# Optimization experiments

Hardware: AMD Instinct MI355X
Metric: run time of the kernel (lower is better)

The kernel has to match this reference:

```python
import jax, jax.numpy as jnp
import numpy as np

B, T, HOR, N = 32, 12, 12, 883
D = 10      # embed_dim == time_dim
HID = 64    # rnn_units
OUT = 1     # output_dim
K = 2       # cheb_k: supports [I, A]


def _pdg2(x, e1, e2, E, Wp, bp):
    # x:[B,N,Ci]  e1,e2:[B,N,D]  E:[N,D]  Wp:[D,K,Ci,Co]  bp:[D,Co]
    nv1 = jnp.tanh(E[None] * e1)                      # [B,N,D]
    nv2 = jnp.tanh(E[None] * e2)
    A = jax.nn.softmax(jax.nn.relu(jnp.einsum('bnd,bmd->bnm', nv1, nv2)), axis=-1)
    xg = jnp.stack([x, jnp.einsum('bnm,bmc->bnc', A, x)], axis=2)   # [B,N,K,Ci]
    W = jnp.einsum('bnd,dkio->bnkio', nv1, Wp)        # node/time-adaptive weights
    b = jnp.einsum('bnd,do->bno', nv1, bp)
    return jnp.einsum('bnki,bnkio->bno', xg, W) + b


def _cell(x, h, e1, e2, E, gW, gb, uW, ub):
    xs = jnp.concatenate([x, h], axis=-1)
    zr = jax.nn.sigmoid(_pdg2(xs, e1, e2, E, gW, gb))
    z, r = jnp.split(zr, 2, axis=-1)
    cand = jnp.concatenate([x, z * h], axis=-1)
    hc = jnp.tanh(_pdg2(cand, e1, e2, E, uW, ub))
    return r * h + (1.0 - r) * hc


def setup_inputs() -> dict:
    key = jax.random.key(0)
    ks = jax.random.split(key, 20)
    s = 0.1
    inp = {
        'src_vals': jax.random.normal(ks[0], (B, T, N, 1), jnp.float32),
        'node_emb': s * jax.random.normal(ks[1], (N, D), jnp.float32),
        'tid_emb1': s * jax.random.normal(ks[2], (288, D), jnp.float32),
        'tid_emb2': s * jax.random.normal(ks[3], (288, D), jnp.float32),
        'diw_emb1': s * jax.random.normal(ks[4], (7, D), jnp.float32),
        'diw_emb2': s * jax.random.normal(ks[5], (7, D), jnp.float32),
        'enc_gate_W': s * jax.random.normal(ks[6], (D, K, 1 + HID, 2 * HID), jnp.float32),
        'enc_gate_b': s * jax.random.normal(ks[7], (D, 2 * HID), jnp.float32),
        'enc_upd_W': s * jax.random.normal(ks[8], (D, K, 1 + HID, HID), jnp.float32),
        'enc_upd_b': s * jax.random.normal(ks[9], (D, HID), jnp.float32),
        'dec_gate_W': s * jax.random.normal(ks[10], (D, K, OUT + HID, 2 * HID), jnp.float32),
        'dec_gate_b': s * jax.random.normal(ks[11], (D, 2 * HID), jnp.float32),
        'dec_upd_W': s * jax.random.normal(ks[12], (D, K, OUT + HID, HID), jnp.float32),
        'dec_upd_b': s * jax.random.normal(ks[13], (D, HID), jnp.float32),
        'proj_W': s * jax.random.normal(ks[14], (OUT, HID), jnp.float32),
        'proj_b': jnp.zeros((OUT,), jnp.float32),
        'src_tid': jax.random.randint(ks[15], (B, T, N), 0, 288, jnp.int32),
        'src_diw': jax.random.randint(ks[16], (B, T, N), 0, 7, jnp.int32),
        'tgt_tid': jax.random.randint(ks[17], (B, HOR, N), 0, 288, jnp.int32),
        'tgt_diw': jax.random.randint(ks[18], (B, HOR, N), 0, 7, jnp.int32),
    }
    return inp


def reference(src_vals, node_emb, tid_emb1, tid_emb2, diw_emb1, diw_emb2,
              enc_gate_W, enc_gate_b, enc_upd_W, enc_upd_b,
              dec_gate_W, dec_gate_b, dec_upd_W, dec_upd_b,
              proj_W, proj_b, src_tid, src_diw, tgt_tid, tgt_diw):
    tm = lambda a: jnp.swapaxes(a, 0, 1)   # batch-major -> time-major
    # periodic embeddings (use_week=True -> elementwise product)
    e1_en = tid_emb1[src_tid] * diw_emb1[src_diw]   # [B,T,N,D]
    e2_en = tid_emb2[src_tid] * diw_emb2[src_diw]
    e1_de = tid_emb1[tgt_tid] * diw_emb1[tgt_diw]   # [B,HOR,N,D]
    e2_de = tid_emb2[tgt_tid] * diw_emb2[tgt_diw]

    h0 = jnp.zeros((src_vals.shape[0], node_emb.shape[0], HID), src_vals.dtype)

    def enc_step(h, inp):
        x, e1, e2 = inp
        h = _cell(x, h, e1, e2, node_emb, enc_gate_W, enc_gate_b, enc_upd_W, enc_upd_b)
        return h, None

    h, _ = jax.lax.scan(enc_step, h0, (tm(src_vals), tm(e1_en), tm(e2_en)))

    go0 = jnp.zeros((src_vals.shape[0], node_emb.shape[0], OUT), src_vals.dtype)

    def dec_step(carry, inp):
        h, go = carry
        e1, e2 = inp
        h = _cell(go, h, e1, e2, node_emb, dec_gate_W, dec_gate_b, dec_upd_W, dec_upd_b)
        go = h @ proj_W.T + proj_b
        return (h, go), go

    _, outs = jax.lax.scan(dec_step, (h, go0), (tm(e1_de), tm(e2_de)))
    return jnp.swapaxes(outs, 0, 1)   # [B,HOR,N,OUT]
```

## Files before the change

kernel.cpp:

```cpp
#include <hip/hip_runtime.h>

#define BB 32
#define TSRC 12
#define HORZ 12
#define NN 883
#define DD 10
#define HH 64
#define BN (BB*NN)
#define BNP 28288
#define KF 5
#define NT 14

typedef __attribute__((ext_vector_type(8))) short short8;
typedef __attribute__((ext_vector_type(4))) float f32x4;

static __device__ __forceinline__ float sigmf(float x) { return 1.f/(1.f + __expf(-x)); }
static __device__ __forceinline__ float tanh_fast(float x) {
  float e = __expf(2.f*x);
  return (e - 1.f) / (e + 1.f);
}
static __device__ __forceinline__ unsigned int bf_hi(float f) {
  unsigned int u = __float_as_uint(f);
  return (u + 0x7fffu + ((u >> 16) & 1u)) >> 16;
}
static __device__ __forceinline__ float bf_f(unsigned int h) {
  return __uint_as_float(h << 16);
}
static __device__ __forceinline__ void lds_load16(const void* g, void* l) {
  __builtin_amdgcn_global_load_lds(
      (const __attribute__((address_space(1))) void*)g,
      (__attribute__((address_space(3))) void*)l, 16, 0, 0);
}

static __device__ __forceinline__ void swz_block(int& b, int& rt) {
  int lin = blockIdx.x + blockIdx.y*NT;
  int c = lin & 7, q = lin >> 3;
  b = c + ((q/NT) << 3);
  rt = q - (q/NT)*NT;
}

static __device__ __forceinline__ void xs_store(unsigned short* chunk, int c, int mm2, float v) {
  int p0 = (c*128 + (mm2 ^ ((c & 7) << 4))) >> 1;
  unsigned int hi = bf_hi(v);
  chunk[p0] = (unsigned short)hi;
  chunk[p0 + 4096] = (unsigned short)bf_hi(v - bf_f(hi));
}

__global__ __launch_bounds__(256) void prep_kernel(
    const float* __restrict__ tidE1, const float* __restrict__ tidE2,
    const float* __restrict__ diwE1, const float* __restrict__ diwE2,
    const float* __restrict__ nodeE,
    const int* __restrict__ tididx, const int* __restrict__ diwidx,
    const float* __restrict__ xsrc, int xmode, int t, int tlen,
    float* __restrict__ nv1T, float* __restrict__ nv2T,
    unsigned short* __restrict__ XsH, unsigned short* __restrict__ XsZ)
{
  int i = blockIdx.x*256 + threadIdx.x;
  if (i >= BN) return;
  int b = i / NN, n = i - b*NN;
  int gi = (b*tlen + t)*NN + n;
  int ti = tididx[gi]*DD, di = diwidx[gi]*DD;
  int nE = n*DD;
#pragma unroll
  for (int d = 0; d < DD; ++d) {
    float E = nodeE[nE+d];
    nv1T[d*BNP+i] = tanh_fast(E * (tidE1[ti+d] * diwE1[di+d]));
    nv2T[d*BNP+i] = tanh_fast(E * (tidE2[ti+d] * diwE2[di+d]));
  }
  float xv = (xmode == 0) ? xsrc[gi] : xsrc[i];
  size_t cb = ((size_t)(b*NT + (n >> 6)))*8192;
  int mm = n & 63;
  unsigned int hi = bf_hi(xv);
  unsigned short los = (unsigned short)bf_hi(xv - bf_f(hi));
  XsH[cb + mm] = (unsigned short)hi; XsH[cb + 4096 + mm] = los;
  XsZ[cb + mm] = (unsigned short)hi; XsZ[cb + 4096 + mm] = los;
}

__global__ __launch_bounds__(256) void wsplit_kernel(
    const float* __restrict__ W, const float* __restrict__ bias,
    int NO, unsigned short* __restrict__ Wf)
{
  int i = blockIdx.x*256 + threadIdx.x;
  int total = DD*2*KF*4*NO*8;
  if (i >= total) return;
  int j = i & 7; int r = i >> 3;
  int o = r % NO; r /= NO;
  int quad = r & 3; r >>= 2;
  int kf = r % KF; r /= KF;
  int hl = r & 1; int d = r >> 1;
  int kk = kf*32 + quad*8 + j;
  float v = 0.f;
  if (kk <= 64)       v = W[(size_t)(d*130 + kk)*NO + o];
  else if (kk == 65)  v = bias[d*NO + o];
  else if (kk <= 130) v = W[(size_t)(d*130 + kk - 1)*NO + o];
  unsigned int hi = bf_hi(v);
  Wf[i] = (hl == 0) ? (unsigned short)hi : (unsigned short)bf_hi(v - bf_f(hi));
}


__global__ __launch_bounds__(256,3) void attn_gate(
    const float* __restrict__ nv1T, const float* __restrict__ nv2T,
    const unsigned short* __restrict__ Xs,
    const float* __restrict__ hsrc,
    const float* __restrict__ xsrc, int xmode, int t, int tlen,
    const unsigned short* __restrict__ Wf,
    float* __restrict__ zh, float* __restrict__ rbuf,
    unsigned short* __restrict__ XsZ)
{
  __shared__ float nv1s[DD][64];
  __shared__ float linv[64];
  __shared__ alignas(16) unsigned char U[46080];
  unsigned short* XT = (unsigned short*)U;
  unsigned short* PT = (unsigned short*)(U + 16384);
  float* nv2s = (float*)(U + 34816);
  float* xcolb = (float*)(U + 39936);
  int b, rt;
  swz_block(b, rt);
  int r0 = rt*64;
  int tid = threadIdx.x;
  int rg = tid >> 4, cg = tid & 15;
  int base = b*NN;
  int lane = tid & 63, lm = lane & 15, quad = lane >> 4;
  int w = tid >> 6, mp = w >> 1, np = w & 1;
  const unsigned short* XsB = Xs + (size_t)b*NT*8192;

  for (int idx = tid; idx < DD*64; idx += 256) {
    int d = idx >> 6, r = idx & 63;
    nv1s[d][r] = (r0 + r < NN) ? nv1T[d*BNP + base + r0 + r] : 0.f;
  }

  int4 xt[4];
  float nvr[3]; float xcr;
  {
    const int4* s0 = (const int4*)XsB;
#pragma unroll
    for (int i = 0; i < 4; ++i) xt[i] = s0[w*64 + lane + i*256];
#pragma unroll
    for (int i = 0; i < 3; ++i) {
      int idx = tid + i*256; float v = 0.f;
      if (idx < DD*64) { int d = idx>>6, m = idx&63; v = (m < NN) ? nv2T[d*BNP + base + m] : 0.f; }
      nvr[i] = v;
    }
    xcr = (tid < 64 && tid < NN) ? hsrc[(size_t)63*BNP + base + tid] : 0.f;
#pragma unroll
    for (int i = 0; i < 4; ++i)
      *(int4*)((char*)XT + w*1024 + lane*16 + i*4096) = xt[i];
#pragma unroll
    for (int i = 0; i < 3; ++i) {
      int idx = tid + i*256;
      if (idx < DD*64) nv2s[idx] = nvr[i];
    }
    if (tid < 64) xcolb[tid] = xcr;
  }
  __syncthreads();

  f32x4 accv[2][2] = {};
  float acclp[4] = {}, acc5p[4] = {};

  for (int tI = 0; tI < NT; ++tI) {
    int cur = tI & 1, nxt = cur ^ 1;
    int m0 = tI*64, m0n = m0 + 64;
    bool hasn = tI < NT-1;
    if (hasn) {
      const int4* src = (const int4*)(XsB + (size_t)(tI+1)*8192);
#pragma unroll
      for (int i = 0; i < 4; ++i) xt[i] = src[w*64 + lane + i*256];
#pragma unroll
      for (int i = 0; i < 3; ++i) {
        int idx = tid + i*256; float v = 0.f;
        if (idx < DD*64) { int d = idx>>6, m = idx&63; v = (m0n + m < NN) ? nv2T[d*BNP + base + m0n + m] : 0.f; }
        nvr[i] = v;
      }
      xcr = (tid < 64 && m0n + tid < NN) ? hsrc[(size_t)63*BNP + base + m0n + tid] : 0.f;
    }
    float s[4][4] = {};
#pragma unroll
    for (int d = 0; d < DD; ++d) {
      float4 a4 = *(const float4*)&nv1s[d][rg*4];
      float4 c4 = *(const float4*)&nv2s[cur*(DD*64) + d*64 + cg*4];
      const float* ap = (const float*)&a4;
      const float* cp = (const float*)&c4;
#pragma unroll
      for (int j = 0; j < 4; ++j)
#pragma unroll
        for (int jj = 0; jj < 4; ++jj)
          s[j][jj] += ap[j]*cp[jj];
    }
    int mvlim = NN - m0;
    float ev[4][4];
#pragma unroll
    for (int jj = 0; jj < 4; ++jj) {
      int m = cg*4 + jj;
      float xm = xcolb[cur*64 + m];
      bool okm = m < mvlim;
#pragma unroll
      for (int j = 0; j < 4; ++j) {
        float e = okm ? __expf(fmaxf(s[j][jj], 0.f)) : 0.f;
        ev[j][jj] = e;
        acclp[j] += e;
        acc5p[j] = fmaf(e, xm, acc5p[j]);
      }
    }
    {
      unsigned int* P1 = (unsigned int*)PT;
      unsigned int* P2 = (unsigned int*)(PT + 64*72);
#pragma unroll
      for (int j = 0; j < 4; ++j) {
        int r = rg*4 + j;
        unsigned int h0 = bf_hi(ev[j][0]), h1 = bf_hi(ev[j][1]), h2 = bf_hi(ev[j][2]), h3 = bf_hi(ev[j][3]);
        unsigned int l0 = bf_hi(ev[j][0]-bf_f(h0)), l1 = bf_hi(ev[j][1]-bf_f(h1));
        unsigned int l2 = bf_hi(ev[j][2]-bf_f(h2)), l3 = bf_hi(ev[j][3]-bf_f(h3));
        int dw = r*36 + cg*2;
        P1[dw] = h0 | (h1 << 16); P1[dw+1] = h2 | (h3 << 16);
        P2[dw] = l0 | (l1 << 16); P2[dw+1] = l2 | (l3 << 16);
      }
    }
    __syncthreads();
    {
      short8 Aa[2][2], Ab[2][2], Ba[2][2], Bb[2][2];
#pragma unroll
      for (int mt = 0; mt < 2; ++mt) {
        int r = mp*32 + mt*16 + lm;
#pragma unroll
        for (int kf = 0; kf < 2; ++kf) {
          Aa[mt][kf] = *(const short8*)&PT[r*72 + quad*8 + kf*32];
          Ab[mt][kf] = *(const short8*)&PT[64*72 + r*72 + quad*8 + kf*32];
        }
      }
#pragma unroll
      for (int ntl = 0; ntl < 2; ++ntl) {
        int c = np*32 + ntl*16 + lm;
        int swz = (c & 7) << 4;
        int cb0 = c*128 + quad*16;
#pragma unroll
        for (int kf = 0; kf < 2; ++kf) {
          int a = (cb0 + kf*64) ^ swz;
          Ba[ntl][kf] = *(const short8*)((const char*)XT + a);
          Bb[ntl][kf] = *(const short8*)((const char*)XT + a + 8192);
        }
      }
#pragma unroll
      for (int kf = 0; kf < 2; ++kf)
#pragma unroll
        for (int mt = 0; mt < 2; ++mt)
#pragma unroll
          for (int ntl = 0; ntl < 2; ++ntl) {
            accv[mt][ntl] = __builtin_amdgcn_mfma_f32_16x16x32_bf16(Aa[mt][kf], Ba[ntl][kf], accv[mt][ntl], 0,0,0);
            accv[mt][ntl] = __builtin_amdgcn_mfma_f32_16x16x32_bf16(Aa[mt][kf], Bb[ntl][kf], accv[mt][ntl], 0,0,0);
            accv[mt][ntl] = __builtin_amdgcn_mfma_f32_16x16x32_bf16(Ab[mt][kf], Ba[ntl][kf], accv[mt][ntl], 0,0,0);
          }
    }
    if (hasn) {
#pragma unroll
      for (int i = 0; i < 3; ++i) {
        int idx = tid + i*256;
        if (idx < DD*64) nv2s[nxt*(DD*64) + idx] = nvr[i];
      }
      if (tid < 64) xcolb[nxt*64 + tid] = xcr;
    }
    __syncthreads();
    if (hasn) {
#pragma unroll
      for (int i = 0; i < 4; ++i)
        *(int4*)((char*)XT + w*1024 + lane*16 + i*4096) = xt[i];
    }
  }
  int mrow_x = tid >> 2, ksub = tid & 3;
  int gmx = base + r0 + mrow_x;
  float hv0[9], hv1[9];
  {
    bool nok = (r0 + mrow_x) < NN;
    float xv;
    if (xmode == 0) xv = nok ? xsrc[(b*tlen+t)*NN + r0 + mrow_x] : 0.f;
    else xv = xsrc[gmx];
#pragma unroll
    for (int i = 0; i < 9; ++i) {
      int kk = ksub*2 + 8*i;
      if (kk > 64) { hv0[i] = 0.f; hv1[i] = 0.f; continue; }
      hv0[i] = (kk == 0) ? xv : hsrc[(size_t)(kk-1)*BNP + gmx];
      hv1[i] = (kk == 64) ? 1.f : hsrc[(size_t)kk*BNP + gmx];
    }
  }
#pragma unroll
  for (int off = 1; off <= 8; off <<= 1)
#pragma unroll
    for (int j = 0; j < 4; ++j) {
      acclp[j] += __shfl_xor(acclp[j], off, 64);
      acc5p[j] += __shfl_xor(acc5p[j], off, 64);
    }
  __syncthreads();
  {
    unsigned int* Z = (unsigned int*)(U + 36864);
    for (int idx = tid; idx < 2304; idx += 256) Z[idx] = 0;
  }
  __syncthreads();
  unsigned short* XA = (unsigned short*)U;
  if (cg == 0) {
#pragma unroll
    for (int j = 0; j < 4; ++j) {
      float li = 1.f / acclp[j];
      int r = rg*4 + j;
      linv[r] = li;
      float v = acc5p[j]*li;
      unsigned int hi = bf_hi(v);
      XA[(4*64 + r)*72 + 2] = (unsigned short)hi;
      XA[(4*64 + r)*72 + 32 + 2] = (unsigned short)bf_hi(v - bf_f(hi));
    }
  }
  __syncthreads();
#pragma unroll
  for (int mt = 0; mt < 2; ++mt) {
    int rbase = mp*32 + mt*16 + quad*4;
    float4 lv = *(const float4*)&linv[rbase];
    const float* lvp = (const float*)&lv;
#pragma unroll
    for (int ntl = 0; ntl < 2; ++ntl) {
      int c = np*32 + ntl*16 + lm;
      int kk = 66 + c;
      int kf = kk >> 5, kkl = kk & 31;
#pragma unroll
      for (int r4 = 0; r4 < 4; ++r4) {
        float v = accv[mt][ntl][r4] * lvp[r4];
        unsigned int hi = bf_hi(v);
        int p = (kf*64 + rbase + r4)*72 + kkl;
        XA[p] = (unsigned short)hi;
        XA[p + 32] = (unsigned short)bf_hi(v - bf_f(hi));
      }
    }
  }
  {
    unsigned int* X1 = (unsigned int*)U;
#pragma unroll
    for (int i = 0; i < 9; ++i) {
      int kk = ksub*2 + 8*i;
      if (kk > 64) continue;
      float v0 = hv0[i], v1 = hv1[i];
      unsigned int h0 = bf_hi(v0), h1 = bf_hi(v1);
      unsigned int l0 = bf_hi(v0 - bf_f(h0)), l1 = bf_hi(v1 - bf_f(h1));
      int kf = kk >> 5, kkl = kk & 31;
      int dw = (kf*64 + mrow_x)*36 + (kkl >> 1);
      X1[dw] = h0 | (h1 << 16);
      X1[dw + 16] = l0 | (l1 << 16);
    }
  }
  __syncthreads();
  short8 A1[2][KF], A2[2][KF];
#pragma unroll
  for (int mt = 0; mt < 2; ++mt) {
    int mrow = mp*32 + mt*16 + lm;
#pragma unroll
    for (int kf = 0; kf < KF; ++kf) {
      A1[mt][kf] = *(const short8*)&XA[(kf*64 + mrow)*72 + quad*8];
      A2[mt][kf] = *(const short8*)&XA[(kf*64 + mrow)*72 + 32 + quad*8];
    }
  }
  __syncthreads();
  unsigned char* bufA = U;
  unsigned char* bufB = U + 20480;
  const int colb = np*32 + lm;
#pragma unroll 1
  for (int co = 0; co < 2; ++co) {
    int co0 = co*64;
    {
      const unsigned short* src = Wf + ((size_t)(w*5)*128 + co0)*8 + lane*8;
#pragma unroll
      for (int i = 0; i < 5; ++i)
        lds_load16(src + (size_t)i*128*8, bufA + (w*5+i)*1024);
    }
    f32x4 accO[2][2] = {};
#pragma unroll 1
    for (int d = 0; d < DD; ++d) {
      f32x4 td[2][2] = {};
      __syncthreads();
      {
        const unsigned short* src = Wf + ((size_t)((d*2+1)*20 + w*5)*128 + co0)*8 + lane*8;
#pragma unroll
        for (int i = 0; i < 5; ++i)
          lds_load16(src + (size_t)i*128*8, bufB + (w*5+i)*1024);
      }
#pragma unroll
      for (int kf = 0; kf < KF; ++kf) {
        int cb = ((kf*4 + quad)*64 + colb)*16;
#pragma unroll
        for (int ntl = 0; ntl < 2; ++ntl) {
          short8 Bh = *(const short8*)(bufA + cb + ntl*256);
          td[0][ntl] = __builtin_amdgcn_mfma_f32_16x16x32_bf16(A1[0][kf], Bh, td[0][ntl], 0,0,0);
          td[0][ntl] = __builtin_amdgcn_mfma_f32_16x16x32_bf16(A2[0][kf], Bh, td[0][ntl], 0,0,0);
          td[1][ntl] = __builtin_amdgcn_mfma_f32_16x16x32_bf16(A1[1][kf], Bh, td[1][ntl], 0,0,0);
          td[1][ntl] = __builtin_amdgcn_mfma_f32_16x16x32_bf16(A2[1][kf], Bh, td[1][ntl], 0,0,0);
        }
      }
      __syncthreads();
      if (d < DD-1) {
        const unsigned short* src = Wf + ((size_t)((d+1)*2*20 + w*5)*128 + co0)*8 + lane*8;
#pragma unroll
        for (int i = 0; i < 5; ++i)
          lds_load16(src + (size_t)i*128*8, bufA + (w*5+i)*1024);
      }
#pragma unroll
      for (int kf = 0; kf < KF; ++kf) {
        int cb = ((kf*4 + quad)*64 + colb)*16;
#pragma unroll
        for (int ntl = 0; ntl < 2; ++ntl) {
          short8 Bl = *(const short8*)(bufB + cb + ntl*256);
          td[0][ntl] = __builtin_amdgcn_mfma_f32_16x16x32_bf16(A1[0][kf], Bl, td[0][ntl], 0,0,0);
          td[1][ntl] = __builtin_amdgcn_mfma_f32_16x16x32_bf16(A1[1][kf], Bl, td[1][ntl], 0,0,0);
        }
      }
#pragma unroll
      for (int mt = 0; mt < 2; ++mt) {
        float4 nv4 = *(const float4*)&nv1s[d][mp*32 + mt*16 + quad*4];
        const float* nvp = (const float*)&nv4;
#pragma unroll
        for (int ntl = 0; ntl < 2; ++ntl)
#pragma unroll
          for (int r = 0; r < 4; ++r)
            accO[mt][ntl][r] += nvp[r] * td[mt][ntl][r];
      }
    }
    float* CT = (float*)U;
    __syncthreads();
#pragma unroll
    for (int mt = 0; mt < 2; ++mt)
#pragma unroll
      for (int ntl = 0; ntl < 2; ++ntl)
#pragma unroll
        for (int r = 0; r < 4; ++r)
          CT[(mp*32 + mt*16 + quad*4 + r)*67 + np*32 + ntl*16 + lm] = accO[mt][ntl][r];
    __syncthreads();
    {
      int mm = tid & 63, og = tid >> 6;
      int n = r0 + mm;
      int gm = base + n;
      bool okn = n < NN;
      if (co == 0) {
        unsigned short* chk = XsZ + ((size_t)(b*NT + rt))*8192;
        int mm2 = mm*2;
        for (int j = 0; j < 16; ++j) {
          int o = og*16 + j;
          float z = sigmf(CT[mm*67 + o]);
          float zhv = z * hsrc[(size_t)o*BNP + gm];
          if (okn) {
            zh[(size_t)o*BNP + gm] = zhv;
            if (o < 63) xs_store(chk, o + 1, mm2, zhv);
          }
        }
      } else {
        for (int j = 0; j < 16; ++j) {
          int o = og*16 + j;
          if (okn) rbuf[(size_t)o*BNP + gm] = sigmf(CT[mm*67 + o]);
        }
      }
    }
    __syncthreads();
  }
}

__global__ __launch_bounds__(256,3) void attn_upd(
    const float* __restrict__ nv1T, const float* __restrict__ nv2T,
    const unsigned short* __restrict__ Xs,
    const float* __restrict__ hsrc,
    const float* __restrict__ hstate,
    const float* __restrict__ xsrc, int xmode, int t, int tlen,
    const unsigned short* __restrict__ Wf,
    const float* __restrict__ rbuf,
    int dec, const float* __restrict__ pW, const float* __restrict__ pb,
    float* __restrict__ go, float* __restrict__ dout,
    unsigned short* __restrict__ XsH)
{
  __shared__ float nv1s[DD][64];
  __shared__ float linv[64];
  __shared__ alignas(16) unsigned char U[46080];
  unsigned short* XT = (unsigned short*)U;
  unsigned short* PT = (unsigned short*)(U + 16384);
  float* nv2s = (float*)(U + 34816);
  float* xcolb = (float*)(U + 39936);
  int b, rt;
  swz_block(b, rt);
  int r0 = rt*64;
  int tid = threadIdx.x;
  int rg = tid >> 4, cg = tid & 15;
  int base = b*NN;
  int lane = tid & 63, lm = lane & 15, quad = lane >> 4;
  int w = tid >> 6, mp = w >> 1, np = w & 1;
  const unsigned short* XsB = Xs + (size_t)b*NT*8192;

  for (int idx = tid; idx < DD*64; idx += 256) {
    int d = idx >> 6, r = idx & 63;
    nv1s[d][r] = (r0 + r < NN) ? nv1T[d*BNP + base + r0 + r] : 0.f;
  }

  int4 xt[4];
  float nvr[3]; float xcr;
  {
    const int4* s0 = (const int4*)XsB;
#pragma unroll
    for (int i = 0; i < 4; ++i) xt[i] = s0[w*64 + lane + i*256];
#pragma unroll
    for (int i = 0; i < 3; ++i) {
      int idx = tid + i*256; float v = 0.f;
      if (idx < DD*64) { int d = idx>>6, m = idx&63; v = (m < NN) ? nv2T[d*BNP + base + m] : 0.f; }
      nvr[i] = v;
    }
    xcr = (tid < 64 && tid < NN) ? hsrc[(size_t)63*BNP + base + tid] : 0.f;
#pragma unroll
    for (int i = 0; i < 4; ++i)
      *(int4*)((char*)XT + w*1024 + lane*16 + i*4096) = xt[i];
#pragma unroll
    for (int i = 0; i < 3; ++i) {
      int idx = tid + i*256;
      if (idx < DD*64) nv2s[idx] = nvr[i];
    }
    if (tid < 64) xcolb[tid] = xcr;
  }
  __syncthreads();

  f32x4 accv[2][2] = {};
  float acclp[4] = {}, acc5p[4] = {};

  for (int tI = 0; tI < NT; ++tI) {
    int cur = tI & 1, nxt = cur ^ 1;
    int m0 = tI*64, m0n = m0 + 64;
    bool hasn = tI < NT-1;
    if (hasn) {
      const int4* src = (const int4*)(XsB + (size_t)(tI+1)*8192);
#pragma unroll
      for (int i = 0; i < 4; ++i) xt[i] = src[w*64 + lane + i*256];
#pragma unroll
      for (int i = 0; i < 3; ++i) {
        int idx = tid + i*256; float v = 0.f;
        if (idx < DD*64) { int d = idx>>6, m = idx&63; v = (m0n + m < NN) ? nv2T[d*BNP + base + m0n + m] : 0.f; }
        nvr[i] = v;
      }
      xcr = (tid < 64 && m0n + tid < NN) ? hsrc[(size_t)63*BNP + base + m0n + tid] : 0.f;
    }
    float s[4][4] = {};
#pragma unroll
    for (int d = 0; d < DD; ++d) {
      float4 a4 = *(const float4*)&nv1s[d][rg*4];
      float4 c4 = *(const float4*)&nv2s[cur*(DD*64) + d*64 + cg*4];
      const float* ap = (const float*)&a4;
      const float* cp = (const float*)&c4;
#pragma unroll
      for (int j = 0; j < 4; ++j)
#pragma unroll
        for (int jj = 0; jj < 4; ++jj)
          s[j][jj] += ap[j]*cp[jj];
    }
    int mvlim = NN - m0;
    float ev[4][4];
#pragma unroll
    for (int jj = 0; jj < 4; ++jj) {
      int m = cg*4 + jj;
      float xm = xcolb[cur*64 + m];
      bool okm = m < mvlim;
#pragma unroll
      for (int j = 0; j < 4; ++j) {
        float e = okm ? __expf(fmaxf(s[j][jj], 0.f)) : 0.f;
        ev[j][jj] = e;
        acclp[j] += e;
        acc5p[j] = fmaf(e, xm, acc5p[j]);
      }
    }
    {
      unsigned int* P1 = (unsigned int*)PT;
      unsigned int* P2 = (unsigned int*)(PT + 64*72);
#pragma unroll
      for (int j = 0; j < 4; ++j) {
        int r = rg*4 + j;
        unsigned int h0 = bf_hi(ev[j][0]), h1 = bf_hi(ev[j][1]), h2 = bf_hi(ev[j][2]), h3 = bf_hi(ev[j][3]);
        unsigned int l0 = bf_hi(ev[j][0]-bf_f(h0)), l1 = bf_hi(ev[j][1]-bf_f(h1));
        unsigned int l2 = bf_hi(ev[j][2]-bf_f(h2)), l3 = bf_hi(ev[j][3]-bf_f(h3));
        int dw = r*36 + cg*2;
        P1[dw] = h0 | (h1 << 16); P1[dw+1] = h2 | (h3 << 16);
        P2[dw] = l0 | (l1 << 16); P2[dw+1] = l2 | (l3 << 16);
      }
    }
    __syncthreads();
    {
      short8 Aa[2][2], Ab[2][2], Ba[2][2], Bb[2][2];
#pragma unroll
      for (int mt = 0; mt < 2; ++mt) {
        int r = mp*32 + mt*16 + lm;
#pragma unroll
        for (int kf = 0; kf < 2; ++kf) {
          Aa[mt][kf] = *(const short8*)&PT[r*72 + quad*8 + kf*32];
          Ab[mt][kf] = *(const short8*)&PT[64*72 + r*72 + quad*8 + kf*32];
        }
      }
#pragma unroll
      for (int ntl = 0; ntl < 2; ++ntl) {
        int c = np*32 + ntl*16 + lm;
        int swz = (c & 7) << 4;
        int cb0 = c*128 + quad*16;
#pragma unroll
        for (int kf = 0; kf < 2; ++kf) {
          int a = (cb0 + kf*64) ^ swz;
          Ba[ntl][kf] = *(const short8*)((const char*)XT + a);
          Bb[ntl][kf] = *(const short8*)((const char*)XT + a + 8192);
        }
      }
#pragma unroll
      for (int kf = 0; kf < 2; ++kf)
#pragma unroll
        for (int mt = 0; mt < 2; ++mt)
#pragma unroll
          for (int ntl = 0; ntl < 2; ++ntl) {
            accv[mt][ntl] = __builtin_amdgcn_mfma_f32_16x16x32_bf16(Aa[mt][kf], Ba[ntl][kf], accv[mt][ntl], 0,0,0);
            accv[mt][ntl] = __builtin_amdgcn_mfma_f32_16x16x32_bf16(Aa[mt][kf], Bb[ntl][kf], accv[mt][ntl], 0,0,0);
            accv[mt][ntl] = __builtin_amdgcn_mfma_f32_16x16x32_bf16(Ab[mt][kf], Ba[ntl][kf], accv[mt][ntl], 0,0,0);
          }
    }
    if (hasn) {
#pragma unroll
      for (int i = 0; i < 3; ++i) {
        int idx = tid + i*256;
        if (idx < DD*64) nv2s[nxt*(DD*64) + idx] = nvr[i];
      }
      if (tid < 64) xcolb[nxt*64 + tid] = xcr;
    }
    __syncthreads();
    if (hasn) {
#pragma unroll
      for (int i = 0; i < 4; ++i)
        *(int4*)((char*)XT + w*1024 + lane*16 + i*4096) = xt[i];
    }
  }
  int mrow_x = tid >> 2, ksub = tid & 3;
  int gmx = base + r0 + mrow_x;
  float hv0[9], hv1[9];
  {
    bool nok = (r0 + mrow_x) < NN;
    float xv;
    if (xmode == 0) xv = nok ? xsrc[(b*tlen+t)*NN + r0 + mrow_x] : 0.f;
    else xv = xsrc[gmx];
#pragma unroll
    for (int i = 0; i < 9; ++i) {
      int kk = ksub*2 + 8*i;
      if (kk > 64) { hv0[i] = 0.f; hv1[i] = 0.f; continue; }
      hv0[i] = (kk == 0) ? xv : hsrc[(size_t)(kk-1)*BNP + gmx];
      hv1[i] = (kk == 64) ? 1.f : hsrc[(size_t)kk*BNP + gmx];
    }
  }
#pragma unroll
  for (int off = 1; off <= 8; off <<= 1)
#pragma unroll
    for (int j = 0; j < 4; ++j) {
      acclp[j] += __shfl_xor(acclp[j], off, 64);
      acc5p[j] += __shfl_xor(acc5p[j], off, 64);
    }
  __syncthreads();
  {
    unsigned int* Z = (unsigned int*)(U + 36864);
    for (int idx = tid; idx < 2304; idx += 256) Z[idx] = 0;
  }
  __syncthreads();
  unsigned short* XA = (unsigned short*)U;
  if (cg == 0) {
#pragma unroll
    for (int j = 0; j < 4; ++j) {
      float li = 1.f / acclp[j];
      int r = rg*4 + j;
      linv[r] = li;
      float v = acc5p[j]*li;
      unsigned int hi = bf_hi(v);
      XA[(4*64 + r)*72 + 2] = (unsigned short)hi;
      XA[(4*64 + r)*72 + 32 + 2] = (unsigned short)bf_hi(v - bf_f(hi));
    }
  }
  __syncthreads();
#pragma unroll
  for (int mt = 0; mt < 2; ++mt) {
    int rbase = mp*32 + mt*16 + quad*4;
    float4 lv = *(const float4*)&linv[rbase];
    const float* lvp = (const float*)&lv;
#pragma unroll
    for (int ntl = 0; ntl < 2; ++ntl) {
      int c = np*32 + ntl*16 + lm;
      int kk = 66 + c;
      int kf = kk >> 5, kkl = kk & 31;
#pragma unroll
      for (int r4 = 0; r4 < 4; ++r4) {
        float v = accv[mt][ntl][r4] * lvp[r4];
        unsigned int hi = bf_hi(v);
        int p = (kf*64 + rbase + r4)*72 + kkl;
        XA[p] = (unsigned short)hi;
        XA[p + 32] = (unsigned short)bf_hi(v - bf_f(hi));
      }
    }
  }
  {
    unsigned int* X1 = (unsigned int*)U;
#pragma unroll
    for (int i = 0; i < 9; ++i) {
      int kk = ksub*2 + 8*i;
      if (kk > 64) continue;
      float v0 = hv0[i], v1 = hv1[i];
      unsigned int h0 = bf_hi(v0), h1 = bf_hi(v1);
      unsigned int l0 = bf_hi(v0 - bf_f(h0)), l1 = bf_hi(v1 - bf_f(h1));
      int kf = kk >> 5, kkl = kk & 31;
      int dw = (kf*64 + mrow_x)*36 + (kkl >> 1);
      X1[dw] = h0 | (h1 << 16);
      X1[dw + 16] = l0 | (l1 << 16);
    }
  }
  __syncthreads();
  short8 A1[2][KF], A2[2][KF];
#pragma unroll
  for (int mt = 0; mt < 2; ++mt) {
    int mrow = mp*32 + mt*16 + lm;
#pragma unroll
    for (int kf = 0; kf < KF; ++kf) {
      A1[mt][kf] = *(const short8*)&XA[(kf*64 + mrow)*72 + quad*8];
      A2[mt][kf] = *(const short8*)&XA[(kf*64 + mrow)*72 + 32 + quad*8];
    }
  }
  __syncthreads();
  unsigned char* bufA = U;
  unsigned char* bufB = U + 20480;
  const int colb = np*32 + lm;
  {
    const unsigned short* src = Wf + (size_t)(w*5)*64*8 + lane*8;
#pragma unroll
    for (int i = 0; i < 5; ++i)
      lds_load16(src + (size_t)i*64*8, bufA + (w*5+i)*1024);
  }
  f32x4 accO[2][2] = {};
#pragma unroll 1
  for (int d = 0; d < DD; ++d) {
    f32x4 td[2][2] = {};
    __syncthreads();
    {
      const unsigned short* src = Wf + (size_t)((d*2+1)*20 + w*5)*64*8 + lane*8;
#pragma unroll
      for (int i = 0; i < 5; ++i)
        lds_load16(src + (size_t)i*64*8, bufB + (w*5+i)*1024);
    }
#pragma unroll
    for (int kf = 0; kf < KF; ++kf) {
      int cb = ((kf*4 + quad)*64 + colb)*16;
#pragma unroll
      for (int ntl = 0; ntl < 2; ++ntl) {
        short8 Bh = *(const short8*)(bufA + cb + ntl*256);
        td[0][ntl] = __builtin_amdgcn_mfma_f32_16x16x32_bf16(A1[0][kf], Bh, td[0][ntl], 0,0,0);
        td[0][ntl] = __builtin_amdgcn_mfma_f32_16x16x32_bf16(A2[0][kf], Bh, td[0][ntl], 0,0,0);
        td[1][ntl] = __builtin_amdgcn_mfma_f32_16x16x32_bf16(A1[1][kf], Bh, td[1][ntl], 0,0,0);
        td[1][ntl] = __builtin_amdgcn_mfma_f32_16x16x32_bf16(A2[1][kf], Bh, td[1][ntl], 0,0,0);
      }
    }
    __syncthreads();
    if (d < DD-1) {
      const unsigned short* src = Wf + (size_t)((d+1)*2*20 + w*5)*64*8 + lane*8;
#pragma unroll
      for (int i = 0; i < 5; ++i)
        lds_load16(src + (size_t)i*64*8, bufA + (w*5+i)*1024);
    }
#pragma unroll
    for (int kf = 0; kf < KF; ++kf) {
      int cb = ((kf*4 + quad)*64 + colb)*16;
#pragma unroll
      for (int ntl = 0; ntl < 2; ++ntl) {
        short8 Bl = *(const short8*)(bufB + cb + ntl*256);
        td[0][ntl] = __builtin_amdgcn_mfma_f32_16x16x32_bf16(A1[0][kf], Bl, td[0][ntl], 0,0,0);
        td[1][ntl] = __builtin_amdgcn_mfma_f32_16x16x32_bf16(A1[1][kf], Bl, td[1][ntl], 0,0,0);
      }
    }
#pragma unroll
    for (int mt = 0; mt < 2; ++mt) {
      float4 nv4 = *(const float4*)&nv1s[d][mp*32 + mt*16 + quad*4];
      const float* nvp = (const float*)&nv4;
#pragma unroll
      for (int ntl = 0; ntl < 2; ++ntl)
#pragma unroll
        for (int r = 0; r < 4; ++r)
          accO[mt][ntl][r] += nvp[r] * td[mt][ntl][r];
    }
  }
  float* CT = (float*)U;
  __syncthreads();
#pragma unroll
  for (int mt = 0; mt < 2; ++mt)
#pragma unroll
    for (int ntl = 0; ntl < 2; ++ntl)
#pragma unroll
      for (int r = 0; r < 4; ++r)
        CT[(mp*32 + mt*16 + quad*4 + r)*67 + np*32 + ntl*16 + lm] = accO[mt][ntl][r];
  __syncthreads();
  {
    int mm = tid & 63, og = tid >> 6;
    int n = r0 + mm;
    int gm = base + n;
    bool okn = n < NN;
    unsigned short* chk = XsH + ((size_t)(b*NT + rt))*8192;
    int mm2 = mm*2;
    float pp = 0.f;
    for (int j = 0; j < 16; ++j) {
      int o = og*16 + j;
      float hc = tanhf(CT[mm*67 + o]);
      float r = rbuf[(size_t)o*BNP + gm];
      float hv = hstate[(size_t)o*BNP + gm];
      float hn = r*hv + (1.f - r)*hc;
      if (okn) {
        ((float*)hstate)[(size_t)o*BNP + gm] = hn;
        if (o < 63) xs_store(chk, o + 1, mm2, hn);
      }
      if (dec) pp = fmaf(hn, pW[o], pp);
    }
    if (dec) {
      float* PS = CT + 64*67;
      __syncthreads();
      PS[mm*4 + og] = pp;
      __syncthreads();
      if (tid < 64) {
        int n2 = r0 + tid;
        if (n2 < NN) {
          float s = pb[0] + PS[tid*4] + PS[tid*4+1] + PS[tid*4+2] + PS[tid*4+3];
          go[base + n2] = s;
          dout[(b*HORZ + t)*NN + n2] = s;
        }
      }
    }
  }
}

extern "C" void kernel_launch(void* const* d_in, const int* in_sizes, int n_in,
                              void* d_out, int out_size, void* d_ws, size_t ws_size,
                              hipStream_t stream) {
  (void)in_sizes; (void)n_in; (void)out_size; (void)ws_size;
  const float* src_vals = (const float*)d_in[0];
  const float* node_emb = (const float*)d_in[1];
  const float* tid1 = (const float*)d_in[2];
  const float* tid2 = (const float*)d_in[3];
  const float* diw1 = (const float*)d_in[4];
  const float* diw2 = (const float*)d_in[5];
  const float* egW = (const float*)d_in[6];
  const float* egb = (const float*)d_in[7];
  const float* euW = (const float*)d_in[8];
  const float* eub = (const float*)d_in[9];
  const float* dgW = (const float*)d_in[10];
  const float* dgb = (const float*)d_in[11];
  const float* duW = (const float*)d_in[12];
  const float* dub = (const float*)d_in[13];
  const float* pW  = (const float*)d_in[14];
  const float* pb  = (const float*)d_in[15];
  const int* stid = (const int*)d_in[16];
  const int* sdiw = (const int*)d_in[17];
  const int* ttid = (const int*)d_in[18];
  const int* tdiw = (const int*)d_in[19];
  float* out = (float*)d_out;

  float* wp = (float*)d_ws;
  float* hbuf = wp; wp += (size_t)64*BNP;
  float* zh   = wp; wp += (size_t)64*BNP;
  float* rbuf = wp; wp += (size_t)64*BNP;
  float* nv1T = wp; wp += (size_t)DD*BNP;
  float* nv2T = wp; wp += (size_t)DD*BNP;
  float* go   = wp; wp += BN + 64;
  unsigned short* egS = (unsigned short*)wp; wp += 204800;
  unsigned short* dgS = (unsigned short*)wp; wp += 204800;
  unsigned short* euS = (unsigned short*)wp; wp += 102400;
  unsigned short* duS = (unsigned short*)wp; wp += 102400;
  unsigned short* XsH = (unsigned short*)wp; wp += 1835008;
  unsigned short* XsZ = (unsigned short*)wp; wp += 1835008;

  hipMemsetAsync(hbuf, 0, sizeof(float)*(size_t)64*BNP, stream);
  hipMemsetAsync(go, 0, sizeof(float)*(BN+64), stream);
  hipMemsetAsync(XsH, 0, (size_t)BB*NT*16384, stream);
  hipMemsetAsync(XsZ, 0, (size_t)BB*NT*16384, stream);

  wsplit_kernel<<<1600,256,0,stream>>>(egW, egb, 128, egS);
  wsplit_kernel<<<1600,256,0,stream>>>(dgW, dgb, 128, dgS);
  wsplit_kernel<<<800,256,0,stream>>>(euW, eub, 64, euS);
  wsplit_kernel<<<800,256,0,stream>>>(duW, dub, 64, duS);

  dim3 fgrid(NT, BB);
  for (int t = 0; t < TSRC; ++t) {
    prep_kernel<<<111,256,0,stream>>>(tid1,tid2,diw1,diw2,node_emb,stid,sdiw,src_vals,0,t,TSRC,nv1T,nv2T,XsH,XsZ);
    attn_gate<<<fgrid,256,0,stream>>>(nv1T,nv2T,XsH,hbuf,src_vals,0,t,TSRC,egS,zh,rbuf,XsZ);
    attn_upd<<<fgrid,256,0,stream>>>(nv1T,nv2T,XsZ,zh,hbuf,src_vals,0,t,TSRC,euS,rbuf,0,pW,pb,go,out,XsH);
  }
  for (int t = 0; t < HORZ; ++t) {
    prep_kernel<<<111,256,0,stream>>>(tid1,tid2,diw1,diw2,node_emb,ttid,tdiw,go,1,t,HORZ,nv1T,nv2T,XsH,XsZ);
    attn_gate<<<fgrid,256,0,stream>>>(nv1T,nv2T,XsH,hbuf,go,1,t,HORZ,dgS,zh,rbuf,XsZ);
    attn_upd<<<fgrid,256,0,stream>>>(nv1T,nv2T,XsZ,zh,hbuf,go,1,t,HORZ,duS,rbuf,1,pW,pb,go,out,XsH);
  }
}
```

Before: 4.482 ms.

## Split gate output halves across grid z and reuse pre-split bf16 inputs

The gate kernel now launches with a third grid dimension of 2, so each block computes only one 64-column half of the gate output (z or r) rather than looping over both. This doubles the block count for more parallelism, at the cost of repeating the attention/aggregation phase in both blocks. Both kernels now read the hi/lo bf16 input columns directly from the pre-swizzled Xs chunk buffers instead of reloading fp32 hidden state and re-splitting it. The full zh buffer is reduced to just the last column (zh63), and the x/t arguments are dropped from the gate kernel.

```diff
diff --git a/kernel.cpp b/kernel.cpp
--- a/kernel.cpp
+++ b/kernel.cpp
@@ -101,11 +101,374 @@
 __global__ __launch_bounds__(256,3) void attn_gate(
     const float* __restrict__ nv1T, const float* __restrict__ nv2T,
     const unsigned short* __restrict__ Xs,
-    const float* __restrict__ hsrc,
-    const float* __restrict__ xsrc, int xmode, int t, int tlen,
+    const float* __restrict__ h,
     const unsigned short* __restrict__ Wf,
-    float* __restrict__ zh, float* __restrict__ rbuf,
-    unsigned short* __restrict__ XsZ)
+    float* __restrict__ rbuf,
+    unsigned short* __restrict__ XsZ, float* __restrict__ zh63)
+{
+  __shared__ float nv1s[DD][64];
+  __shared__ float linv[64];
+  __shared__ alignas(16) unsigned char U[46080];
+  unsigned short* XT = (unsigned short*)U;
+  unsigned short* PT = (unsigned short*)(U + 16384);
+  float* nv2s = (float*)(U + 34816);
+  float* xcolb = (float*)(U + 39936);
+  int b, rt;
+  swz_block(b, rt);
+  int cz = blockIdx.z;
+  int r0 = rt*64;
+  int tid = threadIdx.x;
+  int rg = tid >> 4, cg = tid & 15;
+  int base = b*NN;
+  int lane = tid & 63, lm = lane & 15, quad = lane >> 4;
+  int w = tid >> 6, mp = w >> 1, np = w & 1;
+  const unsigned short* XsB = Xs + (size_t)b*NT*8192;
+
+  for (int idx = tid; idx < DD*64; idx += 256) {
+    int d = idx >> 6, r = idx & 63;
+    nv1s[d][r] = (r0 + r < NN) ? nv1T[d*BNP + base + r0 + r] : 0.f;
+  }
+
+  int4 xt[4];
+  float nvr[3]; float xcr;
+  {
+    const int4* s0 = (const int4*)XsB;
+#pragma unroll
+    for (int i = 0; i < 4; ++i) xt[i] = s0[w*64 + lane + i*256];
+#pragma unroll
+    for (int i = 0; i < 3; ++i) {
+      int idx = tid + i*256; float v = 0.f;
+      if (idx < DD*64) { int d = idx>>6, m = idx&63; v = (m < NN) ? nv2T[d*BNP + base + m] : 0.f; }
+      nvr[i] = v;
+    }
+    xcr = (tid < 64 && tid < NN) ? h[(size_t)63*BNP + base + tid] : 0.f;
+#pragma unroll
+    for (int i = 0; i < 4; ++i)
+      *(int4*)((char*)XT + w*1024 + lane*16 + i*4096) = xt[i];
+#pragma unroll
+    for (int i = 0; i < 3; ++i) {
+      int idx = tid + i*256;
+      if (idx < DD*64) nv2s[idx] = nvr[i];
+    }
+    if (tid < 64) xcolb[tid] = xcr;
+  }
+  __syncthreads();
+
+  f32x4 accv[2][2] = {};
+  float acclp[4] = {}, acc5p[4] = {};
+
+  for (int tI = 0; tI < NT; ++tI) {
+    int cur = tI & 1, nxt = cur ^ 1;
+    int m0 = tI*64, m0n = m0 + 64;
+    bool hasn = tI < NT-1;
+    if (hasn) {
+      const int4* src = (const int4*)(XsB + (size_t)(tI+1)*8192);
+#pragma unroll
+      for (int i = 0; i < 4; ++i) xt[i] = src[w*64 + lane + i*256];
+#pragma unroll
+      for (int i = 0; i < 3; ++i) {
+        int idx = tid + i*256; float v = 0.f;
+        if (idx < DD*64) { int d = idx>>6, m = idx&63; v = (m0n + m < NN) ? nv2T[d*BNP + base + m0n + m] : 0.f; }
+        nvr[i] = v;
+      }
+      xcr = (tid < 64 && m0n + tid < NN) ? h[(size_t)63*BNP + base + m0n + tid] : 0.f;
+    }
+    float s[4][4] = {};
+#pragma unroll
+    for (int d = 0; d < DD; ++d) {
+      float4 a4 = *(const float4*)&nv1s[d][rg*4];
+      float4 c4 = *(const float4*)&nv2s[cur*(DD*64) + d*64 + cg*4];
+      const float* ap = (const float*)&a4;
+      const float* cp = (const float*)&c4;
+#pragma unroll
+      for (int j = 0; j < 4; ++j)
+#pragma unroll
+        for (int jj = 0; jj < 4; ++jj)
+          s[j][jj] += ap[j]*cp[jj];
+    }
+    int mvlim = NN - m0;
+    float ev[4][4];
+#pragma unroll
+    for (int jj = 0; jj < 4; ++jj) {
+      int m = cg*4 + jj;
+      float xm = xcolb[cur*64 + m];
+      bool okm = m < mvlim;
+#pragma unroll
+      for (int j = 0; j < 4; ++j) {
+        float e = okm ? __expf(fmaxf(s[j][jj], 0.f)) : 0.f;
+        ev[j][jj] = e;
+        acclp[j] += e;
+        acc5p[j] = fmaf(e, xm, acc5p[j]);
+      }
+    }
+    {
+      unsigned int* P1 = (unsigned int*)PT;
+      unsigned int* P2 = (unsigned int*)(PT + 64*72);
+#pragma unroll
+      for (int j = 0; j < 4; ++j) {
+        int r = rg*4 + j;
+        unsigned int h0 = bf_hi(ev[j][0]), h1 = bf_hi(ev[j][1]), h2 = bf_hi(ev[j][2]), h3 = bf_hi(ev[j][3]);
+        unsigned int l0 = bf_hi(ev[j][0]-bf_f(h0)), l1 = bf_hi(ev[j][1]-bf_f(h1));
+        unsigned int l2 = bf_hi(ev[j][2]-bf_f(h2)), l3 = bf_hi(ev[j][3]-bf_f(h3));
+        int dw = r*36 + cg*2;
+        P1[dw] = h0 | (h1 << 16); P1[dw+1] = h2 | (h3 << 16);
+        P2[dw] = l0 | (l1 << 16); P2[dw+1] = l2 | (l3 << 16);
+      }
+    }
+    __syncthreads();
+    {
+      short8 Aa[2][2], Ab[2][2], Ba[2][2], Bb[2][2];
+#pragma unroll
+      for (int mt = 0; mt < 2; ++mt) {
+        int r = mp*32 + mt*16 + lm;
+#pragma unroll
+        for (int kf = 0; kf < 2; ++kf) {
+          Aa[mt][kf] = *(const short8*)&PT[r*72 + quad*8 + kf*32];
+          Ab[mt][kf] = *(const short8*)&PT[64*72 + r*72 + quad*8 + kf*32];
+        }
+      }
+#pragma unroll
+      for (int ntl = 0; ntl < 2; ++ntl) {
+        int c = np*32 + ntl*16 + lm;
+        int swz = (c & 7) << 4;
+        int cb0 = c*128 + quad*16;
+#pragma unroll
+        for (int kf = 0; kf < 2; ++kf) {
+          int a = (cb0 + kf*64) ^ swz;
+          Ba[ntl][kf] = *(const short8*)((const char*)XT + a);
+          Bb[ntl][kf] = *(const short8*)((const char*)XT + a + 8192);
+        }
+      }
+#pragma unroll
+      for (int kf = 0; kf < 2; ++kf)
+#pragma unroll
+        for (int mt = 0; mt < 2; ++mt)
+#pragma unroll
+          for (int ntl = 0; ntl < 2; ++ntl) {
+            accv[mt][ntl] = __builtin_amdgcn_mfma_f32_16x16x32_bf16(Aa[mt][kf], Ba[ntl][kf], accv[mt][ntl], 0,0,0);
+            accv[mt][ntl] = __builtin_amdgcn_mfma_f32_16x16x32_bf16(Aa[mt][kf], Bb[ntl][kf], accv[mt][ntl], 0,0,0);
+            accv[mt][ntl] = __builtin_amdgcn_mfma_f32_16x16x32_bf16(Ab[mt][kf], Ba[ntl][kf], accv[mt][ntl], 0,0,0);
+          }
+    }
+    if (hasn) {
+#pragma unroll
+      for (int i = 0; i < 3; ++i) {
+        int idx = tid + i*256;
+        if (idx < DD*64) nv2s[nxt*(DD*64) + idx] = nvr[i];
+      }
+      if (tid < 64) xcolb[nxt*64 + tid] = xcr;
+    }
+    __syncthreads();
+    if (hasn) {
+#pragma unroll
+      for (int i = 0; i < 4; ++i)
+        *(int4*)((char*)XT + w*1024 + lane*16 + i*4096) = xt[i];
+    }
+  }
+  int mrow_x = tid >> 2, ksub = tid & 3;
+  int gmx = base + r0 + mrow_x;
+  const unsigned short* chk_in = Xs + (size_t)(b*NT + rt)*8192;
+  int mm2x = mrow_x*2;
+  unsigned int pjh[9], pjl[9];
+  {
+    float r63v = h[(size_t)63*BNP + gmx];
+    unsigned int h63 = bf_hi(r63v);
+    unsigned int l63 = bf_hi(r63v - bf_f(h63));
+#pragma unroll
+    for (int i = 0; i < 9; ++i) {
+      int kk = ksub*2 + 8*i;
+      unsigned int h0 = 0, l0 = 0, h1 = 0, l1 = 0;
+      if (kk <= 63) {
+        int idx = (kk*128 + (mm2x ^ ((kk & 7) << 4))) >> 1;
+        h0 = chk_in[idx]; l0 = chk_in[idx + 4096];
+      } else if (kk == 64) { h0 = h63; l0 = l63; }
+      int k1 = kk + 1;
+      if (kk <= 62) {
+        int idx1 = (k1*128 + (mm2x ^ ((k1 & 7) << 4))) >> 1;
+        h1 = chk_in[idx1]; l1 = chk_in[idx1 + 4096];
+      } else if (k1 == 65) { h1 = 0x3F80u; l1 = 0u; }
+      pjh[i] = h0 | (h1 << 16);
+      pjl[i] = l0 | (l1 << 16);
+    }
+  }
+#pragma unroll
+  for (int off = 1; off <= 8; off <<= 1)
+#pragma unroll
+    for (int j = 0; j < 4; ++j) {
+      acclp[j] += __shfl_xor(acclp[j], off, 64);
+      acc5p[j] += __shfl_xor(acc5p[j], off, 64);
+    }
+  __syncthreads();
+  {
+    unsigned int* Z = (unsigned int*)(U + 36864);
+    for (int idx = tid; idx < 2304; idx += 256) Z[idx] = 0;
+  }
+  __syncthreads();
+  unsigned short* XA = (unsigned short*)U;
+  if (cg == 0) {
+#pragma unroll
+    for (int j = 0; j < 4; ++j) {
+      float li = 1.f / acclp[j];
+      int r = rg*4 + j;
+      linv[r] = li;
+      float v = acc5p[j]*li;
+      unsigned int hi = bf_hi(v);
+      XA[(4*64 + r)*72 + 2] = (unsigned short)hi;
+      XA[(4*64 + r)*72 + 32 + 2] = (unsigned short)bf_hi(v - bf_f(hi));
+    }
+  }
+  __syncthreads();
+#pragma unroll
+  for (int mt = 0; mt < 2; ++mt) {
+    int rbase = mp*32 + mt*16 + quad*4;
+    float4 lv = *(const float4*)&linv[rbase];
+    const float* lvp = (const float*)&lv;
+#pragma unroll
+    for (int ntl = 0; ntl < 2; ++ntl) {
+      int c = np*32 + ntl*16 + lm;
+      int kk = 66 + c;
+      int kf = kk >> 5, kkl = kk & 31;
+#pragma unroll
+      for (int r4 = 0; r4 < 4; ++r4) {
+        float v = accv[mt][ntl][r4] * lvp[r4];
+        unsigned int hi = bf_hi(v);
+        int p = (kf*64 + rbase + r4)*72 + kkl;
+        XA[p] = (unsigned short)hi;
+        XA[p + 32] = (unsigned short)bf_hi(v - bf_f(hi));
+      }
+    }
+  }
+  {
+    unsigned int* X1 = (unsigned int*)U;
+#pragma unroll
+    for (int i = 0; i < 9; ++i) {
+      int kk = ksub*2 + 8*i;
+      if (kk > 64) continue;
+      int kf = kk >> 5, kkl = kk & 31;
+      int dw = (kf*64 + mrow_x)*36 + (kkl >> 1);
+      X1[dw] = pjh[i];
+      X1[dw + 16] = pjl[i];
+    }
+  }
+  __syncthreads();
+  short8 A1[2][KF], A2[2][KF];
+#pragma unroll
+  for (int mt = 0; mt < 2; ++mt) {
+    int mrow = mp*32 + mt*16 + lm;
+#pragma unroll
+    for (int kf = 0; kf < KF; ++kf) {
+      A1[mt][kf] = *(const short8*)&XA[(kf*64 + mrow)*72 + quad*8];
+      A2[mt][kf] = *(const short8*)&XA[(kf*64 + mrow)*72 + 32 + quad*8];
+    }
+  }
+  __syncthreads();
+  unsigned char* bufA = U;
+  unsigned char* bufB = U + 20480;
+  const int colb = np*32 + lm;
+  const int co0 = cz*64;
+  {
+    const unsigned short* src = Wf + ((size_t)(w*5)*128 + co0)*8 + lane*8;
+#pragma unroll
+    for (int i = 0; i < 5; ++i)
+      lds_load16(src + (size_t)i*128*8, bufA + (w*5+i)*1024);
+  }
+  f32x4 accO[2][2] = {};
+#pragma unroll 1
+  for (int d = 0; d < DD; ++d) {
+    f32x4 td[2][2] = {};
+    __syncthreads();
+    {
+      const unsigned short* src = Wf + ((size_t)((d*2+1)*20 + w*5)*128 + co0)*8 + lane*8;
+#pragma unroll
+      for (int i = 0; i < 5; ++i)
+        lds_load16(src + (size_t)i*128*8, bufB + (w*5+i)*1024);
+    }
+#pragma unroll
+    for (int kf = 0; kf < KF; ++kf) {
+      int cb = ((kf*4 + quad)*64 + colb)*16;
+#pragma unroll
+      for (int ntl = 0; ntl < 2; ++ntl) {
+        short8 Bh = *(const short8*)(bufA + cb + ntl*256);
+        td[0][ntl] = __builtin_amdgcn_mfma_f32_16x16x32_bf16(A1[0][kf], Bh, td[0][ntl], 0,0,0);
+        td[0][ntl] = __builtin_amdgcn_mfma_f32_16x16x32_bf16(A2[0][kf], Bh, td[0][ntl], 0,0,0);
+        td[1][ntl] = __builtin_amdgcn_mfma_f32_16x16x32_bf16(A1[1][kf], Bh, td[1][ntl], 0,0,0);
+        td[1][ntl] = __builtin_amdgcn_mfma_f32_16x16x32_bf16(A2[1][kf], Bh, td[1][ntl], 0,0,0);
+      }
+    }
+    __syncthreads();
+    if (d < DD-1) {
+      const unsigned short* src = Wf + ((size_t)((d+1)*2*20 + w*5)*128 + co0)*8 + lane*8;
+#pragma unroll
+      for (int i = 0; i < 5; ++i)
+        lds_load16(src + (size_t)i*128*8, bufA + (w*5+i)*1024);
+    }
+#pragma unroll
+    for (int kf = 0; kf < KF; ++kf) {
+      int cb = ((kf*4 + quad)*64 + colb)*16;
+#pragma unroll
+      for (int ntl = 0; ntl < 2; ++ntl) {
+        short8 Bl = *(const short8*)(bufB + cb + ntl*256);
+        td[0][ntl] = __builtin_amdgcn_mfma_f32_16x16x32_bf16(A1[0][kf], Bl, td[0][ntl], 0,0,0);
+        td[1][ntl] = __builtin_amdgcn_mfma_f32_16x16x32_bf16(A1[1][kf], Bl, td[1][ntl], 0,0,0);
+      }
+    }
+#pragma unroll
+    for (int mt = 0; mt < 2; ++mt) {
+      float4 nv4 = *(const float4*)&nv1s[d][mp*32 + mt*16 + quad*4];
+      const float* nvp = (const float*)&nv4;
+#pragma unroll
+      for (int ntl = 0; ntl < 2; ++ntl)
+#pragma unroll
+        for (int r = 0; r < 4; ++r)
+          accO[mt][ntl][r] += nvp[r] * td[mt][ntl][r];
+    }
+  }
+  float* CT = (float*)U;
+  __syncthreads();
+#pragma unroll
+  for (int mt = 0; mt < 2; ++mt)
+#pragma unroll
+    for (int ntl = 0; ntl < 2; ++ntl)
+#pragma unroll
+      for (int r = 0; r < 4; ++r)
+        CT[(mp*32 + mt*16 + quad*4 + r)*67 + np*32 + ntl*16 + lm] = accO[mt][ntl][r];
+  __syncthreads();
+  {
+    int mm = tid & 63, og = tid >> 6;
+    int n = r0 + mm;
+    int gm = base + n;
+    bool okn = n < NN;
+    if (cz == 0) {
+      unsigned short* chk = XsZ + ((size_t)(b*NT + rt))*8192;
+      int mm2 = mm*2;
+      for (int j = 0; j < 16; ++j) {
+        int o = og*16 + j;
+        float z = sigmf(CT[mm*67 + o]);
+        float zhv = z * h[(size_t)o*BNP + gm];
+        if (okn) {
+          if (o < 63) xs_store(chk, o + 1, mm2, zhv);
+          else zh63[gm] = zhv;
+        }
+      }
+    } else {
+      for (int j = 0; j < 16; ++j) {
+        int o = og*16 + j;
+        if (okn) rbuf[(size_t)o*BNP + gm] = sigmf(CT[mm*67 + o]);
+      }
+    }
+  }
+}
+
+__global__ __launch_bounds__(256,3) void attn_upd(
+    const float* __restrict__ nv1T, const float* __restrict__ nv2T,
+    const unsigned short* __restrict__ Xs,
+    const float* __restrict__ zh63,
+    float* __restrict__ hstate,
+    const unsigned short* __restrict__ Wf,
+    const float* __restrict__ rbuf,
+    int dec, const float* __restrict__ pW, const float* __restrict__ pb,
+    float* __restrict__ go, float* __restrict__ dout,
+    unsigned short* __restrict__ XsH, int t)
 {
   __shared__ float nv1s[DD][64];
   __shared__ float linv[64];
@@ -141,7 +504,7 @@
       if (idx < DD*64) { int d = idx>>6, m = idx&63; v = (m < NN) ? nv2T[d*BNP + base + m] : 0.f; }
       nvr[i] = v;
     }
-    xcr = (tid < 64 && tid < NN) ? hsrc[(size_t)63*BNP + base + tid] : 0.f;
+    xcr = (tid < 64 && tid < NN) ? zh63[base + tid] : 0.f;
 #pragma unroll
     for (int i = 0; i < 4; ++i)
       *(int4*)((char*)XT + w*1024 + lane*16 + i*4096) = xt[i];
@@ -171,7 +534,7 @@
         if (idx < DD*64) { int d = idx>>6, m = idx&63; v = (m0n + m < NN) ? nv2T[d*BNP + base + m0n + m] : 0.f; }
         nvr[i] = v;
       }
-      xcr = (tid < 64 && m0n + tid < NN) ? hsrc[(size_t)63*BNP + base + m0n + tid] : 0.f;
+      xcr = (tid < 64 && m0n + tid < NN) ? zh63[base + m0n + tid] : 0.f;
     }
     float s[4][4] = {};
 #pragma unroll
@@ -267,18 +630,28 @@
   }
   int mrow_x = tid >> 2, ksub = tid & 3;
   int gmx = base + r0 + mrow_x;
-  float hv0[9], hv1[9];
-  {
-    bool nok = (r0 + mrow_x) < NN;
-    float xv;
-    if (xmode == 0) xv = nok ? xsrc[(b*tlen+t)*NN + r0 + mrow_x] : 0.f;
-    else xv = xsrc[gmx];
+  const unsigned short* chk_in = Xs + (size_t)(b*NT + rt)*8192;
+  int mm2x = mrow_x*2;
+  unsigned int pjh[9], pjl[9];
+  {
+    float r63v = zh63[gmx];
+    unsigned int h63 = bf_hi(r63v);
+    unsigned int l63 = bf_hi(r63v - bf_f(h63));
 #pragma unroll
     for (int i = 0; i < 9; ++i) {
       int kk = ksub*2 + 8*i;
-      if (kk > 64) { hv0[i] = 0.f; hv1[i] = 0.f; continue; }
-      hv0[i] = (kk == 0) ? xv : hsrc[(size_t)(kk-1)*BNP + gmx];
-      hv1[i] = (kk == 64) ? 1.f : hsrc[(size_t)kk*BNP + gmx];
+      unsigned int h0 = 0, l0 = 0, h1 = 0, l1 = 0;
+      if (kk <= 63) {
+        int idx = (kk*128 + (mm2x ^ ((kk & 7) << 4))) >> 1;
+        h0 = chk_in[idx]; l0 = chk_in[idx + 4096];
+      } else if (kk == 64) { h0 = h63; l0 = l63; }
+      int k1 = kk + 1;
+      if (kk <= 62) {
+        int idx1 = (k1*128 + (mm2x ^ ((k1 & 7) << 4))) >> 1;
+        h1 = chk_in[idx1]; l1 = chk_in[idx1 + 4096];
+      } else if (k1 == 65) { h1 = 0x3F80u; l1 = 0u; }
+      pjh[i] = h0 | (h1 << 16);
+      pjl[i] = l0 | (l1 << 16);
     }
   }
 #pragma unroll
@@ -334,374 +707,10 @@
     for (int i = 0; i < 9; ++i) {
       int kk = ksub*2 + 8*i;
       if (kk > 64) continue;
-      float v0 = hv0[i], v1 = hv1[i];
-      unsigned int h0 = bf_hi(v0), h1 = bf_hi(v1);
-      unsigned int l0 = bf_hi(v0 - bf_f(h0)), l1 = bf_hi(v1 - bf_f(h1));
       int kf = kk >> 5, kkl = kk & 31;
       int dw = (kf*64 + mrow_x)*36 + (kkl >> 1);
-      X1[dw] = h0 | (h1 << 16);
-      X1[dw + 16] = l0 | (l1 << 16);
-    }
-  }
-  __syncthreads();
-  short8 A1[2][KF], A2[2][KF];
-#pragma unroll
-  for (int mt = 0; mt < 2; ++mt) {
-    int mrow = mp*32 + mt*16 + lm;
-#pragma unroll
-    for (int kf = 0; kf < KF; ++kf) {
-      A1[mt][kf] = *(const short8*)&XA[(kf*64 + mrow)*72 + quad*8];
-      A2[mt][kf] = *(const short8*)&XA[(kf*64 + mrow)*72 + 32 + quad*8];
-    }
-  }
-  __syncthreads();
-  unsigned char* bufA = U;
-  unsigned char* bufB = U + 20480;
-  const int colb = np*32 + lm;
-#pragma unroll 1
-  for (int co = 0; co < 2; ++co) {
-    int co0 = co*64;
-    {
-      const unsigned short* src = Wf + ((size_t)(w*5)*128 + co0)*8 + lane*8;
-#pragma unroll
-      for (int i = 0; i < 5; ++i)
-        lds_load16(src + (size_t)i*128*8, bufA + (w*5+i)*1024);
-    }
-    f32x4 accO[2][2] = {};
-#pragma unroll 1
-    for (int d = 0; d < DD; ++d) {
-      f32x4 td[2][2] = {};
-      __syncthreads();
-      {
-        const unsigned short* src = Wf + ((size_t)((d*2+1)*20 + w*5)*128 + co0)*8 + lane*8;
-#pragma unroll
-        for (int i = 0; i < 5; ++i)
-          lds_load16(src + (size_t)i*128*8, bufB + (w*5+i)*1024);
-      }
-#pragma unroll
-      for (int kf = 0; kf < KF; ++kf) {
-        int cb = ((kf*4 + quad)*64 + colb)*16;
-#pragma unroll
-        for (int ntl = 0; ntl < 2; ++ntl) {
-          short8 Bh = *(const short8*)(bufA + cb + ntl*256);
-          td[0][ntl] = __builtin_amdgcn_mfma_f32_16x16x32_bf16(A1[0][kf], Bh, td[0][ntl], 0,0,0);
-          td[0][ntl] = __builtin_amdgcn_mfma_f32_16x16x32_bf16(A2[0][kf], Bh, td[0][ntl], 0,0,0);
-          td[1][ntl] = __builtin_amdgcn_mfma_f32_16x16x32_bf16(A1[1][kf], Bh, td[1][ntl], 0,0,0);
-          td[1][ntl] = __builtin_amdgcn_mfma_f32_16x16x32_bf16(A2[1][kf], Bh, td[1][ntl], 0,0,0);
-        }
-      }
-      __syncthreads();
-      if (d < DD-1) {
-        const unsigned short* src = Wf + ((size_t)((d+1)*2*20 + w*5)*128 + co0)*8 + lane*8;
-#pragma unroll
-        for (int i = 0; i < 5; ++i)
-          lds_load16(src + (size_t)i*128*8, bufA + (w*5+i)*1024);
-      }
-#pragma unroll
-      for (int kf = 0; kf < KF; ++kf) {
-        int cb = ((kf*4 + quad)*64 + colb)*16;
-#pragma unroll
-        for (int ntl = 0; ntl < 2; ++ntl) {
-          short8 Bl = *(const short8*)(bufB + cb + ntl*256);
-          td[0][ntl] = __builtin_amdgcn_mfma_f32_16x16x32_bf16(A1[0][kf], Bl, td[0][ntl], 0,0,0);
-          td[1][ntl] = __builtin_amdgcn_mfma_f32_16x16x32_bf16(A1[1][kf], Bl, td[1][ntl], 0,0,0);
-        }
-      }
-#pragma unroll
-      for (int mt = 0; mt < 2; ++mt) {
-        float4 nv4 = *(const float4*)&nv1s[d][mp*32 + mt*16 + quad*4];
-        const float* nvp = (const float*)&nv4;
-#pragma unroll
-        for (int ntl = 0; ntl < 2; ++ntl)
-#pragma unroll
-          for (int r = 0; r < 4; ++r)
-            accO[mt][ntl][r] += nvp[r] * td[mt][ntl][r];
-      }
-    }
-    float* CT = (float*)U;
-    __syncthreads();
-#pragma unroll
-    for (int mt = 0; mt < 2; ++mt)
-#pragma unroll
-      for (int ntl = 0; ntl < 2; ++ntl)
-#pragma unroll
-        for (int r = 0; r < 4; ++r)
-          CT[(mp*32 + mt*16 + quad*4 + r)*67 + np*32 + ntl*16 + lm] = accO[mt][ntl][r];
-    __syncthreads();
-    {
-      int mm = tid & 63, og = tid >> 6;
-      int n = r0 + mm;
-      int gm = base + n;
-      bool okn = n < NN;
-      if (co == 0) {
-        unsigned short* chk = XsZ + ((size_t)(b*NT + rt))*8192;
-        int mm2 = mm*2;
-        for (int j = 0; j < 16; ++j) {
-          int o = og*16 + j;
-          float z = sigmf(CT[mm*67 + o]);
-          float zhv = z * hsrc[(size_t)o*BNP + gm];
-          if (okn) {
-            zh[(size_t)o*BNP + gm] = zhv;
-            if (o < 63) xs_store(chk, o + 1, mm2, zhv);
-          }
-        }
-      } else {
-        for (int j = 0; j < 16; ++j) {
-          int o = og*16 + j;
-          if (okn) rbuf[(size_t)o*BNP + gm] = sigmf(CT[mm*67 + o]);
-        }
-      }
-    }
-    __syncthreads();
-  }
-}
-
-__global__ __launch_bounds__(256,3) void attn_upd(
-    const float* __restrict__ nv1T, const float* __restrict__ nv2T,
-    const unsigned short* __restrict__ Xs,
-    const float* __restrict__ hsrc,
-    const float* __restrict__ hstate,
-    const float* __restrict__ xsrc, int xmode, int t, int tlen,
-    const unsigned short* __restrict__ Wf,
-    const float* __restrict__ rbuf,
-    int dec, const float* __restrict__ pW, const float* __restrict__ pb,
-    float* __restrict__ go, float* __restrict__ dout,
-    unsigned short* __restrict__ XsH)
-{
-  __shared__ float nv1s[DD][64];
-  __shared__ float linv[64];
-  __shared__ alignas(16) unsigned char U[46080];
-  unsigned short* XT = (unsigned short*)U;
-  unsigned short* PT = (unsigned short*)(U + 16384);
-  float* nv2s = (float*)(U + 34816);
-  float* xcolb = (float*)(U + 39936);
-  int b, rt;
-  swz_block(b, rt);
-  int r0 = rt*64;
-  int tid = threadIdx.x;
-  int rg = tid >> 4, cg = tid & 15;
-  int base = b*NN;
-  int lane = tid & 63, lm = lane & 15, quad = lane >> 4;
-  int w = tid >> 6, mp = w >> 1, np = w & 1;
-  const unsigned short* XsB = Xs + (size_t)b*NT*8192;
-
-  for (int idx = tid; idx < DD*64; idx += 256) {
-    int d = idx >> 6, r = idx & 63;
-    nv1s[d][r] = (r0 + r < NN) ? nv1T[d*BNP + base + r0 + r] : 0.f;
-  }
-
-  int4 xt[4];
-  float nvr[3]; float xcr;
-  {
-    const int4* s0 = (const int4*)XsB;
-#pragma unroll
-    for (int i = 0; i < 4; ++i) xt[i] = s0[w*64 + lane + i*256];
-#pragma unroll
-    for (int i = 0; i < 3; ++i) {
-      int idx = tid + i*256; float v = 0.f;
-      if (idx < DD*64) { int d = idx>>6, m = idx&63; v = (m < NN) ? nv2T[d*BNP + base + m] : 0.f; }
-      nvr[i] = v;
-    }
-    xcr = (tid < 64 && tid < NN) ? hsrc[(size_t)63*BNP + base + tid] : 0.f;
-#pragma unroll
-    for (int i = 0; i < 4; ++i)
-      *(int4*)((char*)XT + w*1024 + lane*16 + i*4096) = xt[i];
-#pragma unroll
-    for (int i = 0; i < 3; ++i) {
-      int idx = tid + i*256;
-      if (idx < DD*64) nv2s[idx] = nvr[i];
-    }
-    if (tid < 64) xcolb[tid] = xcr;
-  }
-  __syncthreads();
-
-  f32x4 accv[2][2] = {};
-  float acclp[4] = {}, acc5p[4] = {};
-
-  for (int tI = 0; tI < NT; ++tI) {
-    int cur = tI & 1, nxt = cur ^ 1;
-    int m0 = tI*64, m0n = m0 + 64;
-    bool hasn = tI < NT-1;
-    if (hasn) {
-      const int4* src = (const int4*)(XsB + (size_t)(tI+1)*8192);
-#pragma unroll
-      for (int i = 0; i < 4; ++i) xt[i] = src[w*64 + lane + i*256];
-#pragma unroll
-      for (int i = 0; i < 3; ++i) {
-        int idx = tid + i*256; float v = 0.f;
-        if (idx < DD*64) { int d = idx>>6, m = idx&63; v = (m0n + m < NN) ? nv2T[d*BNP + base + m0n + m] : 0.f; }
-        nvr[i] = v;
-      }
-      xcr = (tid < 64 && m0n + tid < NN) ? hsrc[(size_t)63*BNP + base + m0n + tid] : 0.f;
-    }
-    float s[4][4] = {};
-#pragma unroll
-    for (int d = 0; d < DD; ++d) {
-      float4 a4 = *(const float4*)&nv1s[d][rg*4];
-      float4 c4 = *(const float4*)&nv2s[cur*(DD*64) + d*64 + cg*4];
-      const float* ap = (const float*)&a4;
-      const float* cp = (const float*)&c4;
-#pragma unroll
-      for (int j = 0; j < 4; ++j)
-#pragma unroll
-        for (int jj = 0; jj < 4; ++jj)
-          s[j][jj] += ap[j]*cp[jj];
-    }
-    int mvlim = NN - m0;
-    float ev[4][4];
-#pragma unroll
-    for (int jj = 0; jj < 4; ++jj) {
-      int m = cg*4 + jj;
-      float xm = xcolb[cur*64 + m];
-      bool okm = m < mvlim;
-#pragma unroll
-      for (int j = 0; j < 4; ++j) {
-        float e = okm ? __expf(fmaxf(s[j][jj], 0.f)) : 0.f;
-        ev[j][jj] = e;
-        acclp[j] += e;
-        acc5p[j] = fmaf(e, xm, acc5p[j]);
-      }
-    }
-    {
-      unsigned int* P1 = (unsigned int*)PT;
-      unsigned int* P2 = (unsigned int*)(PT + 64*72);
-#pragma unroll
-      for (int j = 0; j < 4; ++j) {
-        int r = rg*4 + j;
-        unsigned int h0 = bf_hi(ev[j][0]), h1 = bf_hi(ev[j][1]), h2 = bf_hi(ev[j][2]), h3 = bf_hi(ev[j][3]);
-        unsigned int l0 = bf_hi(ev[j][0]-bf_f(h0)), l1 = bf_hi(ev[j][1]-bf_f(h1));
-        unsigned int l2 = bf_hi(ev[j][2]-bf_f(h2)), l3 = bf_hi(ev[j][3]-bf_f(h3));
-        int dw = r*36 + cg*2;
-        P1[dw] = h0 | (h1 << 16); P1[dw+1] = h2 | (h3 << 16);
-        P2[dw] = l0 | (l1 << 16); P2[dw+1] = l2 | (l3 << 16);
-      }
-    }
-    __syncthreads();
-    {
-      short8 Aa[2][2], Ab[2][2], Ba[2][2], Bb[2][2];
-#pragma unroll
-      for (int mt = 0; mt < 2; ++mt) {
-        int r = mp*32 + mt*16 + lm;
-#pragma unroll
-        for (int kf = 0; kf < 2; ++kf) {
-          Aa[mt][kf] = *(const short8*)&PT[r*72 + quad*8 + kf*32];
-          Ab[mt][kf] = *(const short8*)&PT[64*72 + r*72 + quad*8 + kf*32];
-        }
-      }
-#pragma unroll
-      for (int ntl = 0; ntl < 2; ++ntl) {
-        int c = np*32 + ntl*16 + lm;
-        int swz = (c & 7) << 4;
-        int cb0 = c*128 + quad*16;
-#pragma unroll
-        for (int kf = 0; kf < 2; ++kf) {
-          int a = (cb0 + kf*64) ^ swz;
-          Ba[ntl][kf] = *(const short8*)((const char*)XT + a);
-          Bb[ntl][kf] = *(const short8*)((const char*)XT + a + 8192);
-        }
-      }
-#pragma unroll
-      for (int kf = 0; kf < 2; ++kf)
-#pragma unroll
-        for (int mt = 0; mt < 2; ++mt)
-#pragma unroll
-          for (int ntl = 0; ntl < 2; ++ntl) {
-            accv[mt][ntl] = __builtin_amdgcn_mfma_f32_16x16x32_bf16(Aa[mt][kf], Ba[ntl][kf], accv[mt][ntl], 0,0,0);
-            accv[mt][ntl] = __builtin_amdgcn_mfma_f32_16x16x32_bf16(Aa[mt][kf], Bb[ntl][kf], accv[mt][ntl], 0,0,0);
-            accv[mt][ntl] = __builtin_amdgcn_mfma_f32_16x16x32_bf16(Ab[mt][kf], Ba[ntl][kf], accv[mt][ntl], 0,0,0);
-          }
-    }
-    if (hasn) {
-#pragma unroll
-      for (int i = 0; i < 3; ++i) {
-        int idx = tid + i*256;
-        if (idx < DD*64) nv2s[nxt*(DD*64) + idx] = nvr[i];
-      }
-      if (tid < 64) xcolb[nxt*64 + tid] = xcr;
-    }
-    __syncthreads();
-    if (hasn) {
-#pragma unroll
-      for (int i = 0; i < 4; ++i)
-        *(int4*)((char*)XT + w*1024 + lane*16 + i*4096) = xt[i];
-    }
-  }
-  int mrow_x = tid >> 2, ksub = tid & 3;
-  int gmx = base + r0 + mrow_x;
-  float hv0[9], hv1[9];
-  {
-    bool nok = (r0 + mrow_x) < NN;
-    float xv;
-    if (xmode == 0) xv = nok ? xsrc[(b*tlen+t)*NN + r0 + mrow_x] : 0.f;
-    else xv = xsrc[gmx];
-#pragma unroll
-    for (int i = 0; i < 9; ++i) {
-      int kk = ksub*2 + 8*i;
-      if (kk > 64) { hv0[i] = 0.f; hv1[i] = 0.f; continue; }
-      hv0[i] = (kk == 0) ? xv : hsrc[(size_t)(kk-1)*BNP + gmx];
-      hv1[i] = (kk == 64) ? 1.f : hsrc[(size_t)kk*BNP + gmx];
-    }
-  }
-#pragma unroll
-  for (int off = 1; off <= 8; off <<= 1)
-#pragma unroll
-    for (int j = 0; j < 4; ++j) {
-      acclp[j] += __shfl_xor(acclp[j], off, 64);
-      acc5p[j] += __shfl_xor(acc5p[j], off, 64);
-    }
-  __syncthreads();
-  {
-    unsigned int* Z = (unsigned int*)(U + 36864);
-    for (int idx = tid; idx < 2304; idx += 256) Z[idx] = 0;
-  }
-  __syncthreads();
-  unsigned short* XA = (unsigned short*)U;
-  if (cg == 0) {
-#pragma unroll
-    for (int j = 0; j < 4; ++j) {
-      float li = 1.f / acclp[j];
-      int r = rg*4 + j;
-      linv[r] = li;
-      float v = acc5p[j]*li;
-      unsigned int hi = bf_hi(v);
-      XA[(4*64 + r)*72 + 2] = (unsigned short)hi;
-      XA[(4*64 + r)*72 + 32 + 2] = (unsigned short)bf_hi(v - bf_f(hi));
-    }
-  }
-  __syncthreads();
-#pragma unroll
-  for (int mt = 0; mt < 2; ++mt) {
-    int rbase = mp*32 + mt*16 + quad*4;
-    float4 lv = *(const float4*)&linv[rbase];
-    const float* lvp = (const float*)&lv;
-#pragma unroll
-    for (int ntl = 0; ntl < 2; ++ntl) {
-      int c = np*32 + ntl*16 + lm;
-      int kk = 66 + c;
-      int kf = kk >> 5, kkl = kk & 31;
-#pragma unroll
-      for (int r4 = 0; r4 < 4; ++r4) {
-        float v = accv[mt][ntl][r4] * lvp[r4];
-        unsigned int hi = bf_hi(v);
-        int p = (kf*64 + rbase + r4)*72 + kkl;
-        XA[p] = (unsigned short)hi;
-        XA[p + 32] = (unsigned short)bf_hi(v - bf_f(hi));
-      }
-    }
-  }
-  {
-    unsigned int* X1 = (unsigned int*)U;
-#pragma unroll
-    for (int i = 0; i < 9; ++i) {
-      int kk = ksub*2 + 8*i;
-      if (kk > 64) continue;
-      float v0 = hv0[i], v1 = hv1[i];
-      unsigned int h0 = bf_hi(v0), h1 = bf_hi(v1);
-      unsigned int l0 = bf_hi(v0 - bf_f(h0)), l1 = bf_hi(v1 - bf_f(h1));
-      int kf = kk >> 5, kkl = kk & 31;
-      int dw = (kf*64 + mrow_x)*36 + (kkl >> 1);
-      X1[dw] = h0 | (h1 << 16);
-      X1[dw + 16] = l0 | (l1 << 16);
+      X1[dw] = pjh[i];
+      X1[dw + 16] = pjl[i];
     }
   }
   __syncthreads();
@@ -801,7 +810,7 @@
       float hv = hstate[(size_t)o*BNP + gm];
       float hn = r*hv + (1.f - r)*hc;
       if (okn) {
-        ((float*)hstate)[(size_t)o*BNP + gm] = hn;
+        hstate[(size_t)o*BNP + gm] = hn;
         if (o < 63) xs_store(chk, o + 1, mm2, hn);
       }
       if (dec) pp = fmaf(hn, pW[o], pp);
@@ -851,7 +860,7 @@
 
   float* wp = (float*)d_ws;
   float* hbuf = wp; wp += (size_t)64*BNP;
-  float* zh   = wp; wp += (size_t)64*BNP;
+  float* zh63 = wp; wp += BNP + 64;
   float* rbuf = wp; wp += (size_t)64*BNP;
   float* nv1T = wp; wp += (size_t)DD*BNP;
   float* nv2T = wp; wp += (size_t)DD*BNP;
@@ -873,15 +882,16 @@
   wsplit_kernel<<<800,256,0,stream>>>(euW, eub, 64, euS);
   wsplit_kernel<<<800,256,0,stream>>>(duW, dub, 64, duS);
 
-  dim3 fgrid(NT, BB);
+  dim3 ggrid(NT, BB, 2);
+  dim3 ugrid(NT, BB);
   for (int t = 0; t < TSRC; ++t) {
     prep_kernel<<<111,256,0,stream>>>(tid1,tid2,diw1,diw2,node_emb,stid,sdiw,src_vals,0,t,TSRC,nv1T,nv2T,XsH,XsZ);
-    attn_gate<<<fgrid,256,0,stream>>>(nv1T,nv2T,XsH,hbuf,src_vals,0,t,TSRC,egS,zh,rbuf,XsZ);
-    attn_upd<<<fgrid,256,0,stream>>>(nv1T,nv2T,XsZ,zh,hbuf,src_vals,0,t,TSRC,euS,rbuf,0,pW,pb,go,out,XsH);
+    attn_gate<<<ggrid,256,0,stream>>>(nv1T,nv2T,XsH,hbuf,egS,rbuf,XsZ,zh63);
+    attn_upd<<<ugrid,256,0,stream>>>(nv1T,nv2T,XsZ,zh63,hbuf,euS,rbuf,0,pW,pb,go,out,XsH,t);
   }
   for (int t = 0; t < HORZ; ++t) {
     prep_kernel<<<111,256,0,stream>>>(tid1,tid2,diw1,diw2,node_emb,ttid,tdiw,go,1,t,HORZ,nv1T,nv2T,XsH,XsZ);
-    attn_gate<<<fgrid,256,0,stream>>>(nv1T,nv2T,XsH,hbuf,go,1,t,HORZ,dgS,zh,rbuf,XsZ);
-    attn_upd<<<fgrid,256,0,stream>>>(nv1T,nv2T,XsZ,zh,hbuf,go,1,t,HORZ,duS,rbuf,1,pW,pb,go,out,XsH);
-  }
-}
+    attn_gate<<<ggrid,256,0,stream>>>(nv1T,nv2T,XsH,hbuf,dgS,rbuf,XsZ,zh63);
+    attn_upd<<<ugrid,256,0,stream>>>(nv1T,nv2T,XsZ,zh63,hbuf,duS,rbuf,1,pW,pb,go,out,XsH,t);
+  }
+}
```

Result: slower. 4.835 ms (+7.9%).
